# Kernel optimization log

Measured on AMD Instinct MI355X. Metric: run time of the kernel, lower is better.

Reference implementation:

```python
import jax, jax.numpy as jnp
import numpy as np

B, V, P, L, D = 8, 16, 128, 16, 128
PD = L * D  # patch_dim = patch_size * d_model = 2048


def _layernorm(x, g, b, eps=1e-5):
    mu = jnp.mean(x, axis=-1, keepdims=True)
    var = jnp.mean(jnp.square(x - mu), axis=-1, keepdims=True)
    return (x - mu) / jnp.sqrt(var + eps) * g + b


def setup_inputs() -> dict:
    key = jax.random.key(0)
    ks = jax.random.split(key, 24)
    x = jax.random.normal(ks[0], (B, V, P, L, D), jnp.float32)
    m = jax.random.randint(ks[1], (B, V, V), 0, 2) > 0
    var_mask = m & ~jnp.eye(V, dtype=bool)[None]  # keep self-attention unmasked

    def lin_w(k, fan_in, fan_out):
        return jax.random.normal(k, (fan_in, fan_out), jnp.float32) * (1.0 / np.sqrt(fan_in))

    inp = {"x": x, "var_mask": var_mask}
    # Attn_PatchLevel (attn1): query / shared kv / out projections
    inp["w_q1"] = lin_w(ks[2], PD, PD); inp["b_q1"] = jnp.zeros((PD,), jnp.float32)
    inp["w_kv1"] = lin_w(ks[3], PD, PD); inp["b_kv1"] = jnp.zeros((PD,), jnp.float32)
    inp["w_o1"] = lin_w(ks[4], PD, PD); inp["b_o1"] = jnp.zeros((PD,), jnp.float32)
    # Attn_VarLevel (attn2)
    inp["w_q2"] = lin_w(ks[5], PD, PD); inp["b_q2"] = jnp.zeros((PD,), jnp.float32)
    inp["w_kv2"] = lin_w(ks[6], PD, PD); inp["b_kv2"] = jnp.zeros((PD,), jnp.float32)
    inp["w_o2"] = lin_w(ks[7], PD, PD); inp["b_o2"] = jnp.zeros((PD,), jnp.float32)
    # LayerNorms
    inp["g1"] = jnp.ones((PD,), jnp.float32); inp["be1"] = jnp.zeros((PD,), jnp.float32)
    inp["g2"] = jnp.ones((PD,), jnp.float32); inp["be2"] = jnp.zeros((PD,), jnp.float32)
    inp["g3"] = jnp.ones((PD,), jnp.float32); inp["be3"] = jnp.zeros((PD,), jnp.float32)
    # FFN
    inp["w_l1"] = lin_w(ks[8], PD, 4 * PD); inp["b_l1"] = jnp.zeros((4 * PD,), jnp.float32)
    inp["w_l2"] = lin_w(ks[9], 4 * PD, PD); inp["b_l2"] = jnp.zeros((PD,), jnp.float32)
    return inp


def reference(x, var_mask,
              w_q1, b_q1, w_kv1, b_kv1, w_o1, b_o1,
              w_q2, b_q2, w_kv2, b_kv2, w_o2, b_o2,
              g1, be1, g2, be2, g3, be3,
              w_l1, b_l1, w_l2, b_l2):
    b, v, p, l, d = x.shape
    pd = l * d
    scale = 1.0 / np.sqrt(pd)
    x = x.reshape(b, v, p, pd)

    # ---- Attn_PatchLevel (mask=None -> no masking; keys and values share kv_projection) ----
    q = x @ w_q1 + b_q1
    kv = x @ w_kv1 + b_kv1  # keys == values in the original module
    scores = jnp.einsum('bvpd,bvsd->bvps', q, kv)  # [B,V,P,P]
    attn = jax.nn.softmax(scale * scores, axis=-1)  # dropout is identity at eval
    a1 = jnp.einsum('bvps,bvsd->bvpd', attn, kv) @ w_o1 + b_o1
    x = _layernorm(x + a1, g1, be1)

    # ---- Attn_VarLevel over variables, per patch ----
    x = x.transpose(0, 2, 1, 3)  # [B,P,V,PD]
    q = x @ w_q2 + b_q2
    kv = x @ w_kv2 + b_kv2
    scores = jnp.einsum('bpvd,bprd->bpvr', q, kv)  # [B,P,V,V]
    scores = jnp.where(var_mask[:, None, :, :], -jnp.inf, scores)
    attn = jax.nn.softmax(scale * scores, axis=-1)
    a2 = jnp.einsum('bpvr,bprd->bpvd', attn, kv) @ w_o2 + b_o2
    x = _layernorm(x + a2, g2, be2)

    # ---- FFN (torch nn.GELU default = exact erf) ----
    z = jax.nn.gelu(x @ w_l1 + b_l1, approximate=False)
    x = x + z @ w_l2 + b_l2

    x_out = _layernorm(x, g3, be3).transpose(0, 2, 1, 3)  # [B,V,P,PD]
    x_next = x_out.reshape(b, v, p // 2, 2 * l, d)
    return x_out, x_next
```

## Files before the change

kernel.cpp:

```cpp
#include <hip/hip_runtime.h>
#include <math.h>


using u16   = unsigned short;
using f32x4 = __attribute__((ext_vector_type(4))) float;
using bf16x8= __attribute__((ext_vector_type(8))) __bf16;
using u16x8 = __attribute__((ext_vector_type(8))) u16;
using u16x4 = __attribute__((ext_vector_type(4))) u16;

#define NROWS 16384
#define PD    2048
#define MEMBAR asm volatile("" ::: "memory")

__device__ __forceinline__ float bf2f(u16 u) {
    unsigned v = ((unsigned)u) << 16;
    return __builtin_bit_cast(float, v);
}
__device__ __forceinline__ u16 f2bf(float f) {
    unsigned u = __builtin_bit_cast(unsigned, f);
    u += 0x7FFFu + ((u >> 16) & 1u);
    return (u16)(u >> 16);
}
__device__ __forceinline__ void gload_lds16(const void* g, void* l) {
    __builtin_amdgcn_global_load_lds((const __attribute__((address_space(1))) void*)g,
                                     (__attribute__((address_space(3))) void*)l, 16, 0, 0);
}
__device__ __forceinline__ void block_barrier() {
    MEMBAR; __builtin_amdgcn_s_barrier(); MEMBAR;
}

template<int GELU>
__global__ __launch_bounds__(512, 2)
void gemm256(const u16* __restrict__ A, int lda,
             const u16* __restrict__ B, int ldb,
             u16* __restrict__ C1, u16* __restrict__ C2, int ncut, int ldc,
             const float* __restrict__ bias1, const float* __restrict__ bias2,
             int K, int NT, int CM, int CN)
{
    __shared__ __align__(16) char smem[131072];

    const int tid  = threadIdx.x;
    const int wv   = tid >> 6;
    const int wm   = wv >> 2;
    const int wn   = wv & 3;
    const int lane = tid & 63;
    const int fr   = lane & 15;
    const int fks16= (lane >> 4) * 16;
    const int rmask= (fr & 7) << 4;
    const int kb0  = fks16 ^ rmask;
    const int kb1  = (64 + fks16) ^ rmask;

    const int xcd = blockIdx.x & 7;
    const int ii  = blockIdx.x >> 3;
    const int RY  = NT / CN;
    const int mt  = (xcd / RY) * CM + (ii / CN);
    const int nt  = (xcd % RY) * CN + (ii % CN);
    const int m0  = mt * 256;
    const int n0  = nt * 256;

    const int rsub = tid >> 3;
    const int cswE = (((tid & 7) * 16) ^ ((rsub & 7) << 4)) >> 1;
    const int waveByte = wv * 1024;

    auto stage = [&](const u16* mat, int ld, int row0, int k0, int regionByte) {
        const u16* g0 = mat + (size_t)(row0 + rsub) * ld + k0 + cswE;
        gload_lds16(g0,                   smem + regionByte + waveByte);
        gload_lds16(g0 + (size_t)ld * 64, smem + regionByte + 8192 + waveByte);
    };

    const int aRowByte = (wm * 128 + fr) * 128;
    const int bRowByte = (wn * 64 + fr) * 128;

    const int KT = K >> 6;

    stage(A, lda, m0,       0, 0);
    stage(B, ldb, n0,       0, 32768);
    stage(A, lda, m0 + 128, 0, 16384);
    stage(B, ldb, n0 + 128, 0, 49152);
    stage(B, ldb, n0,      64, 98304);
    stage(A, lda, m0,      64, 65536);
    asm volatile("s_waitcnt vmcnt(4)" ::: "memory");
    __builtin_amdgcn_s_barrier();

    bf16x8 a[4][2], b0[2][2], b1[2][2];
    f32x4  acc[8][4] = {};

    for (int t = 0; t < KT; ++t) {
        const int Ab = (t & 1) ? 65536 : 0;
        const int Bb = Ab + 32768;
        const int Ob = Ab ^ 65536;
        const bool s1 = (t + 1 < KT), s2 = (t + 2 < KT);

        #pragma unroll
        for (int mi = 0; mi < 4; ++mi) {
            const int rb = Ab + aRowByte + mi * 2048;
            a[mi][0] = *(const bf16x8*)(smem + rb + kb0);
            a[mi][1] = *(const bf16x8*)(smem + rb + kb1);
        }
        #pragma unroll
        for (int nj = 0; nj < 2; ++nj) {
            const int rb = Bb + bRowByte + nj * 2048;
            b0[nj][0] = *(const bf16x8*)(smem + rb + kb0);
            b0[nj][1] = *(const bf16x8*)(smem + rb + kb1);
        }
        #pragma unroll
        for (int nj = 0; nj < 2; ++nj) {
            const int rb = Bb + bRowByte + 4096 + nj * 2048;
            b1[nj][0] = *(const bf16x8*)(smem + rb + kb0);
            b1[nj][1] = *(const bf16x8*)(smem + rb + kb1);
        }
        if (s1) stage(B, ldb, n0 + 128, (t + 1) << 6, Ob + 49152);
        __builtin_amdgcn_s_barrier();
        __builtin_amdgcn_s_setprio(1);
        #pragma unroll
        for (int mi = 0; mi < 4; ++mi)
            #pragma unroll
            for (int nj = 0; nj < 2; ++nj) {
                acc[mi][nj] = __builtin_amdgcn_mfma_f32_16x16x32_bf16(a[mi][0], b0[nj][0], acc[mi][nj], 0, 0, 0);
                acc[mi][nj] = __builtin_amdgcn_mfma_f32_16x16x32_bf16(a[mi][1], b0[nj][1], acc[mi][nj], 0, 0, 0);
            }
        __builtin_amdgcn_s_setprio(0);
        __builtin_amdgcn_s_barrier();

        if (s1) stage(A, lda, m0 + 128, (t + 1) << 6, Ob + 16384);
        __builtin_amdgcn_s_barrier();
        __builtin_amdgcn_s_setprio(1);
        #pragma unroll
        for (int mi = 0; mi < 4; ++mi)
            #pragma unroll
            for (int nj = 0; nj < 2; ++nj) {
                acc[mi][2 + nj] = __builtin_amdgcn_mfma_f32_16x16x32_bf16(a[mi][0], b1[nj][0], acc[mi][2 + nj], 0, 0, 0);
                acc[mi][2 + nj] = __builtin_amdgcn_mfma_f32_16x16x32_bf16(a[mi][1], b1[nj][1], acc[mi][2 + nj], 0, 0, 0);
            }
        __builtin_amdgcn_s_setprio(0);
        #pragma unroll
        for (int mi = 0; mi < 4; ++mi) {
            const int rb = Ab + aRowByte + 8192 + mi * 2048;
            a[mi][0] = *(const bf16x8*)(smem + rb + kb0);
            a[mi][1] = *(const bf16x8*)(smem + rb + kb1);
        }
        __builtin_amdgcn_s_barrier();

        if (s2) stage(B, ldb, n0, (t + 2) << 6, Bb);
        __builtin_amdgcn_s_barrier();
        __builtin_amdgcn_s_setprio(1);
        #pragma unroll
        for (int mi = 0; mi < 4; ++mi)
            #pragma unroll
            for (int nj = 0; nj < 2; ++nj) {
                acc[4 + mi][nj] = __builtin_amdgcn_mfma_f32_16x16x32_bf16(a[mi][0], b0[nj][0], acc[4 + mi][nj], 0, 0, 0);
                acc[4 + mi][nj] = __builtin_amdgcn_mfma_f32_16x16x32_bf16(a[mi][1], b0[nj][1], acc[4 + mi][nj], 0, 0, 0);
            }
        __builtin_amdgcn_s_setprio(0);
        __builtin_amdgcn_s_barrier();

        if (s2) stage(A, lda, m0, (t + 2) << 6, Ab);
        __builtin_amdgcn_s_barrier();
        __builtin_amdgcn_s_setprio(1);
        #pragma unroll
        for (int mi = 0; mi < 4; ++mi)
            #pragma unroll
            for (int nj = 0; nj < 2; ++nj) {
                acc[4 + mi][2 + nj] = __builtin_amdgcn_mfma_f32_16x16x32_bf16(a[mi][0], b1[nj][0], acc[4 + mi][2 + nj], 0, 0, 0);
                acc[4 + mi][2 + nj] = __builtin_amdgcn_mfma_f32_16x16x32_bf16(a[mi][1], b1[nj][1], acc[4 + mi][2 + nj], 0, 0, 0);
            }
        __builtin_amdgcn_s_setprio(0);
        if (s2) { asm volatile("s_waitcnt vmcnt(4)" ::: "memory"); }
        else    { asm volatile("s_waitcnt vmcnt(0)" ::: "memory"); }
        __builtin_amdgcn_s_barrier();
    }

    u16* Cout; const float* bs; int ncol;
    if (n0 < ncut) { Cout = C1; bs = bias1; ncol = n0; }
    else           { Cout = C2; bs = bias2; ncol = n0 - ncut; }

    block_barrier();
    u16* lsu = (u16*)smem;
    const int lcolB = wn * 64 + fr;
    const int lrowB = wm * 128 + (lane >> 4) * 4;
    #pragma unroll
    for (int nj = 0; nj < 4; ++nj) {
        const int lcol = lcolB + nj * 16;
        const float bb = bs[ncol + lcol];
        #pragma unroll
        for (int mi = 0; mi < 8; ++mi) {
            #pragma unroll
            for (int j = 0; j < 4; ++j) {
                float v = acc[mi][nj][j] + bb;
                if constexpr (GELU) v = 0.5f * v * (1.f + erff(v * 0.70710678118f));
                lsu[(lrowB + mi * 16 + j) * 256 + lcol] = f2bf(v);
            }
        }
    }
    block_barrier();
    const int hp = tid & 31;
    const int r0 = tid >> 5;
    #pragma unroll
    for (int ps = 0; ps < 16; ++ps) {
        const int r = ps * 16 + r0;
        u16x8 v = *(const u16x8*)&lsu[r * 256 + hp * 8];
        *(u16x8*)&Cout[(size_t)(m0 + r) * ldc + ncol + hp * 8] = v;
    }
}

template<int OUTF32, int HASBIAS>
__global__ __launch_bounds__(256, 2)
void gemm_nt(const u16* __restrict__ A, long sAg, int lda,
             const u16* __restrict__ B, long sBg, int ldb,
             void* __restrict__ Cv, long sCg, int ldc,
             const float* __restrict__ bias, int K, float scale)
{
    __shared__ __align__(16) u16 lsA[128 * 32];
    __shared__ __align__(16) u16 lsB[128 * 32];

    const int tid  = threadIdx.x;
    const int w    = tid >> 6;
    const int lane = tid & 63;
    const int m0   = blockIdx.x * 128;
    const int n0   = blockIdx.y * 128;
    A += (long)blockIdx.z * sAg;
    B += (long)blockIdx.z * sBg;

    const int wr = w >> 1, wc = w & 1;
    f32x4 acc[4][4] = {};

    const int srow = lane >> 2;
    const int skc  = (lane & 3) * 8;
    const int rA0  = 32 * w + srow;
    const int rA1  = rA0 + 16;
    const size_t aoff0 = (size_t)(m0 + rA0) * lda + skc;
    const size_t aoff1 = (size_t)(m0 + rA1) * lda + skc;
    const size_t boff0 = (size_t)(n0 + rA0) * ldb + skc;
    const size_t boff1 = (size_t)(n0 + rA1) * ldb + skc;
    u16* lA0 = lsA + 1024 * w;
    u16* lA1 = lA0 + 512;
    u16* lB0 = lsB + 1024 * w;
    u16* lB1 = lB0 + 512;

    const int fr = lane & 15;
    const int fk = (lane >> 4) * 8;

    for (int k0 = 0; k0 < K; k0 += 32) {
        gload_lds16(A + aoff0 + k0, lA0);
        gload_lds16(A + aoff1 + k0, lA1);
        gload_lds16(B + boff0 + k0, lB0);
        gload_lds16(B + boff1 + k0, lB1);
        __syncthreads();

        bf16x8 af[4], bf[4];
        #pragma unroll
        for (int m = 0; m < 4; m++)
            af[m] = *(const bf16x8*)&lsA[(wr * 64 + m * 16 + fr) * 32 + fk];
        #pragma unroll
        for (int n = 0; n < 4; n++)
            bf[n] = *(const bf16x8*)&lsB[(wc * 64 + n * 16 + fr) * 32 + fk];
        #pragma unroll
        for (int m = 0; m < 4; m++)
            #pragma unroll
            for (int n = 0; n < 4; n++)
                acc[m][n] = __builtin_amdgcn_mfma_f32_16x16x32_bf16(af[m], bf[n], acc[m][n], 0, 0, 0);
        __syncthreads();
    }

    float* Cf = (float*)Cv;
    u16*   Cb = (u16*)Cv;
    const int crow0 = m0 + wr * 64 + (lane >> 4) * 4;
    const int ccol0 = n0 + wc * 64 + fr;
    const long cbase = (long)blockIdx.z * sCg;
    #pragma unroll
    for (int n = 0; n < 4; n++) {
        const int col = ccol0 + n * 16;
        float bb = 0.f;
        if constexpr (HASBIAS) bb = bias[col];
        #pragma unroll
        for (int m = 0; m < 4; m++) {
            #pragma unroll
            for (int j = 0; j < 4; j++) {
                const int row = crow0 + m * 16 + j;
                float v = acc[m][n][j] + bb;
                const long idx = cbase + (long)row * ldc + col;
                if constexpr (OUTF32) Cf[idx] = v * scale;
                else                  Cb[idx] = f2bf(v);
            }
        }
    }
}

__global__ __launch_bounds__(256, 1)
void scores_softmax_kernel(const u16* __restrict__ Q, const u16* __restrict__ KVp,
                           u16* __restrict__ P, float scale)
{
    __shared__ __align__(16) u16 lsA[128 * 32];
    __shared__ __align__(16) u16 lsB[128 * 32];
    __shared__ float SL[128][130];

    const int g = blockIdx.x;
    const u16* A = Q   + (size_t)g * 262144;
    const u16* B = KVp + (size_t)g * 262144;

    const int tid  = threadIdx.x;
    const int w    = tid >> 6;
    const int lane = tid & 63;
    const int wr = w >> 1, wc = w & 1;
    f32x4 acc[4][4] = {};

    const int srow = lane >> 2;
    const int skc  = (lane & 3) * 8;
    const int rA0  = 32 * w + srow;
    const int rA1  = rA0 + 16;
    const size_t aoff0 = (size_t)rA0 * 2048 + skc;
    const size_t aoff1 = (size_t)rA1 * 2048 + skc;
    u16* lA0 = lsA + 1024 * w;
    u16* lA1 = lA0 + 512;
    u16* lB0 = lsB + 1024 * w;
    u16* lB1 = lB0 + 512;

    const int fr = lane & 15;
    const int fk = (lane >> 4) * 8;

    for (int k0 = 0; k0 < 2048; k0 += 32) {
        gload_lds16(A + aoff0 + k0, lA0);
        gload_lds16(A + aoff1 + k0, lA1);
        gload_lds16(B + aoff0 + k0, lB0);
        gload_lds16(B + aoff1 + k0, lB1);
        __syncthreads();
        bf16x8 af[4], bf[4];
        #pragma unroll
        for (int m = 0; m < 4; m++)
            af[m] = *(const bf16x8*)&lsA[(wr * 64 + m * 16 + fr) * 32 + fk];
        #pragma unroll
        for (int n = 0; n < 4; n++)
            bf[n] = *(const bf16x8*)&lsB[(wc * 64 + n * 16 + fr) * 32 + fk];
        #pragma unroll
        for (int m = 0; m < 4; m++)
            #pragma unroll
            for (int n = 0; n < 4; n++)
                acc[m][n] = __builtin_amdgcn_mfma_f32_16x16x32_bf16(af[m], bf[n], acc[m][n], 0, 0, 0);
        __syncthreads();
    }

    const int crow0 = wr * 64 + (lane >> 4) * 4;
    const int ccol0 = wc * 64 + fr;
    #pragma unroll
    for (int n = 0; n < 4; n++)
        #pragma unroll
        for (int m = 0; m < 4; m++)
            #pragma unroll
            for (int j = 0; j < 4; j++)
                SL[crow0 + m * 16 + j][ccol0 + n * 16] = acc[m][n][j] * scale;
    __syncthreads();

    unsigned* Pout = (unsigned*)(P + (size_t)g * 16384);
    for (int r = w * 32; r < w * 32 + 32; ++r) {
        const float v0 = SL[r][lane * 2], v1 = SL[r][lane * 2 + 1];
        float mx = fmaxf(v0, v1);
        #pragma unroll
        for (int d = 1; d < 64; d <<= 1) mx = fmaxf(mx, __shfl_xor(mx, d));
        const float e0 = __expf(v0 - mx), e1 = __expf(v1 - mx);
        float sm = e0 + e1;
        #pragma unroll
        for (int d = 1; d < 64; d <<= 1) sm += __shfl_xor(sm, d);
        const float inv = 1.f / sm;
        Pout[r * 64 + lane] = (unsigned)f2bf(e0 * inv) | ((unsigned)f2bf(e1 * inv) << 16);
    }
}

__global__ __launch_bounds__(256)
void wtrans6_kernel(const float* w0, const float* w1, const float* w2,
                    const float* w3, const float* w4, const float* w5,
                    u16* o0, u16* o1, u16* o2, u16* o3, u16* o4, u16* o5)
{
    const float* ins[6]  = {w0, w1, w2, w3, w4, w5};
    u16*         outs[6] = {o0, o1, o2, o3, o4, o5};
    const float* in  = ins[blockIdx.z];
    u16*         out = outs[blockIdx.z];

    __shared__ float tile[32][33];
    const int c0 = blockIdx.x * 32, r0 = blockIdx.y * 32;
    const int tx = threadIdx.x & 31, ty = threadIdx.x >> 5;
    #pragma unroll
    for (int i = ty; i < 32; i += 8)
        tile[i][tx] = in[(size_t)(r0 + i) * 2048 + c0 + tx];
    __syncthreads();
    #pragma unroll
    for (int i = ty; i < 32; i += 8)
        out[(size_t)(c0 + i) * 2048 + r0 + tx] = f2bf(tile[tx][i]);
}

__global__ __launch_bounds__(256)
void wtrans_kernel(const float* __restrict__ in, u16* __restrict__ out, int R, int C)
{
    __shared__ float tile[32][33];
    const int c0 = blockIdx.x * 32, r0 = blockIdx.y * 32;
    const int tx = threadIdx.x & 31, ty = threadIdx.x >> 5;
    #pragma unroll
    for (int i = ty; i < 32; i += 8)
        tile[i][tx] = in[(size_t)(r0 + i) * C + c0 + tx];
    __syncthreads();
    #pragma unroll
    for (int i = ty; i < 32; i += 8)
        out[(size_t)(c0 + i) * R + r0 + tx] = f2bf(tile[tx][i]);
}

__global__ __launch_bounds__(256)
void kvtrans_kernel(const u16* __restrict__ in, u16* __restrict__ out)
{
    __shared__ u16 tile[32][33];
    const int g = blockIdx.z;
    const int n0 = blockIdx.x * 32, m0 = blockIdx.y * 32;
    const int tx = threadIdx.x & 31, ty = threadIdx.x >> 5;
    #pragma unroll
    for (int i = ty; i < 32; i += 8)
        tile[i][tx] = in[(size_t)(g * 128 + m0 + i) * 2048 + n0 + tx];
    __syncthreads();
    #pragma unroll
    for (int i = ty; i < 32; i += 8)
        out[(size_t)g * 262144 + (size_t)(n0 + i) * 128 + m0 + tx] = tile[tx][i];
}

__global__ __launch_bounds__(256)
void cvt_f32_bf16(const float* __restrict__ in, u16* __restrict__ out)
{
    const long i = ((long)blockIdx.x * 256 + threadIdx.x) * 4;
    float4 v = *(const float4*)(in + i);
    u16x4 o;
    o[0] = f2bf(v.x); o[1] = f2bf(v.y); o[2] = f2bf(v.z); o[3] = f2bf(v.w);
    *(u16x4*)(out + i) = o;
}

template<int FINAL, int RESF32>
__global__ __launch_bounds__(256)
void ln_kernel(const void* __restrict__ residv, const u16* __restrict__ add,
               const float* __restrict__ gam, const float* __restrict__ bet,
               u16* __restrict__ xb, float* __restrict__ o1, float* __restrict__ o2)
{
    const long row = blockIdx.x;
    const int  t   = threadIdx.x;
    const long base = row * PD + t * 8;

    u16x8 av = *(const u16x8*)(add + base);
    float y[8];
    if constexpr (RESF32) {
        const float* resid = (const float*)residv;
        float4 r0 = *(const float4*)(resid + base);
        float4 r1 = *(const float4*)(resid + base + 4);
        y[0] = r0.x + bf2f(av[0]); y[1] = r0.y + bf2f(av[1]);
        y[2] = r0.z + bf2f(av[2]); y[3] = r0.w + bf2f(av[3]);
        y[4] = r1.x + bf2f(av[4]); y[5] = r1.y + bf2f(av[5]);
        y[6] = r1.z + bf2f(av[6]); y[7] = r1.w + bf2f(av[7]);
    } else {
        const u16* resid = (const u16*)residv;
        u16x8 rv = *(const u16x8*)(resid + base);
        #pragma unroll
        for (int j = 0; j < 8; j++) y[j] = bf2f(rv[j]) + bf2f(av[j]);
    }

    float s1 = 0.f, s2 = 0.f;
    #pragma unroll
    for (int j = 0; j < 8; j++) { s1 += y[j]; s2 += y[j] * y[j]; }
    #pragma unroll
    for (int d = 1; d < 64; d <<= 1) { s1 += __shfl_xor(s1, d); s2 += __shfl_xor(s2, d); }
    __shared__ float red[8];
    const int w = t >> 6;
    if ((t & 63) == 0) { red[w] = s1; red[4 + w] = s2; }
    __syncthreads();
    s1 = red[0] + red[1] + red[2] + red[3];
    s2 = red[4] + red[5] + red[6] + red[7];
    const float mean = s1 * (1.f / PD);
    const float var  = s2 * (1.f / PD) - mean * mean;
    const float rstd = rsqrtf(var + 1e-5f);

    float4 g0 = *(const float4*)(gam + t * 8);
    float4 g1 = *(const float4*)(gam + t * 8 + 4);
    float4 b0 = *(const float4*)(bet + t * 8);
    float4 b1 = *(const float4*)(bet + t * 8 + 4);
    float gv[8] = {g0.x, g0.y, g0.z, g0.w, g1.x, g1.y, g1.z, g1.w};
    float bv[8] = {b0.x, b0.y, b0.z, b0.w, b1.x, b1.y, b1.z, b1.w};

    float o[8];
    #pragma unroll
    for (int j = 0; j < 8; j++) o[j] = (y[j] - mean) * rstd * gv[j] + bv[j];

    if constexpr (FINAL) {
        float4 p0 = {o[0], o[1], o[2], o[3]}, p1 = {o[4], o[5], o[6], o[7]};
        *(float4*)(o1 + base) = p0; *(float4*)(o1 + base + 4) = p1;
        *(float4*)(o2 + base) = p0; *(float4*)(o2 + base + 4) = p1;
    } else {
        u16x8 ob;
        #pragma unroll
        for (int j = 0; j < 8; j++) ob[j] = f2bf(o[j]);
        *(u16x8*)(xb + base) = ob;
    }
}

__global__ void detect_mask_kernel(const unsigned char* __restrict__ m, int* __restrict__ flag)
{
    __shared__ int s;
    if (threadIdx.x == 0) s = 0;
    __syncthreads();
    int acc = 0;
    for (int i = threadIdx.x; i < 2048; i += 256)
        if (i & 3) acc |= m[i];
    if (acc) atomicOr(&s, 1);
    __syncthreads();
    if (threadIdx.x == 0) *flag = s;
}

__global__ __launch_bounds__(64)
void attn2_kernel(u16* __restrict__ Q, const u16* __restrict__ KV,
                  const void* __restrict__ mask, const int* __restrict__ mflag,
                  float scale)
{
    const int g = blockIdx.x;
    const int b = g >> 7, p = g & 127;
    const int lane = threadIdx.x;

    const size_t groupbase = ((size_t)(b * 16) * 128 + p) * PD;
    const size_t vstride   = (size_t)128 * PD;

    const int am   = lane & 15;
    const int koff = (lane >> 4) * 8;
    const u16* qp = Q  + groupbase + (size_t)am * vstride + koff;
    const u16* kp = KV + groupbase + (size_t)am * vstride + koff;

    f32x4 acc = {0.f, 0.f, 0.f, 0.f};
    for (int k0 = 0; k0 < PD; k0 += 32) {
        bf16x8 a  = *(const bf16x8*)(qp + k0);
        bf16x8 bb = *(const bf16x8*)(kp + k0);
        acc = __builtin_amdgcn_mfma_f32_16x16x32_bf16(a, bb, acc, 0, 0, 0);
    }

    const int vk = lane & 15;
    const int hi = lane >> 4;
    const int mf = *mflag;
    __shared__ float PL[16][16];
    float pv[4];
    #pragma unroll
    for (int j = 0; j < 4; j++) {
        const int vq = hi * 4 + j;
        float s = acc[j] * scale;
        const int midx = b * 256 + vq * 16 + vk;
        int msk;
        if (mf) msk = ((const unsigned char*)mask)[midx];
        else    msk = ((const int*)mask)[midx];
        if (msk) s = -1e30f;
        pv[j] = s;
    }
    #pragma unroll
    for (int j = 0; j < 4; j++) {
        float mx = pv[j];
        #pragma unroll
        for (int d = 1; d < 16; d <<= 1) mx = fmaxf(mx, __shfl_xor(mx, d));
        const float e = __expf(pv[j] - mx);
        float sm = e;
        #pragma unroll
        for (int d = 1; d < 16; d <<= 1) sm += __shfl_xor(sm, d);
        pv[j] = e / sm;
    }
    #pragma unroll
    for (int j = 0; j < 4; j++) PL[hi * 4 + j][vk] = pv[j];
    __syncthreads();

    const u16* kvr[16];
    #pragma unroll
    for (int v = 0; v < 16; v++) kvr[v] = KV + groupbase + (size_t)v * vstride;

    for (int vqt = 0; vqt < 16; vqt += 4) {
        float pr[4][16];
        #pragma unroll
        for (int q = 0; q < 4; q++)
            #pragma unroll
            for (int k = 0; k < 16; k++) pr[q][k] = PL[vqt + q][k];
        u16* o0 = Q + groupbase + (size_t)(vqt + 0) * vstride;
        u16* o1 = Q + groupbase + (size_t)(vqt + 1) * vstride;
        u16* o2 = Q + groupbase + (size_t)(vqt + 2) * vstride;
        u16* o3 = Q + groupbase + (size_t)(vqt + 3) * vstride;
        for (int n0 = 0; n0 < PD; n0 += 64) {
            const int n = n0 + lane;
            float a0 = 0.f, a1 = 0.f, a2 = 0.f, a3 = 0.f;
            #pragma unroll
            for (int k = 0; k < 16; k++) {
                const float kvv = bf2f(kvr[k][n]);
                a0 += pr[0][k] * kvv; a1 += pr[1][k] * kvv;
                a2 += pr[2][k] * kvv; a3 += pr[3][k] * kvv;
            }
            o0[n] = f2bf(a0); o1[n] = f2bf(a1); o2[n] = f2bf(a2); o3[n] = f2bf(a3);
        }
    }
}

extern "C" void kernel_launch(void* const* d_in, const int* in_sizes, int n_in,
                              void* d_out, int out_size, void* d_ws, size_t ws_size,
                              hipStream_t stream)
{
    const float* x0    = (const float*)d_in[0];
    const void*  vmask = d_in[1];
    const float* w_q1  = (const float*)d_in[2];  const float* b_q1  = (const float*)d_in[3];
    const float* w_kv1 = (const float*)d_in[4];  const float* b_kv1 = (const float*)d_in[5];
    const float* w_o1  = (const float*)d_in[6];  const float* b_o1  = (const float*)d_in[7];
    const float* w_q2  = (const float*)d_in[8];  const float* b_q2  = (const float*)d_in[9];
    const float* w_kv2 = (const float*)d_in[10]; const float* b_kv2 = (const float*)d_in[11];
    const float* w_o2  = (const float*)d_in[12]; const float* b_o2  = (const float*)d_in[13];
    const float* g1 = (const float*)d_in[14]; const float* be1 = (const float*)d_in[15];
    const float* g2 = (const float*)d_in[16]; const float* be2 = (const float*)d_in[17];
    const float* g3 = (const float*)d_in[18]; const float* be3 = (const float*)d_in[19];
    const float* w_l1 = (const float*)d_in[20]; const float* b_l1 = (const float*)d_in[21];
    const float* w_l2 = (const float*)d_in[22]; const float* b_l2 = (const float*)d_in[23];

    char* ws = (char*)d_ws;
    size_t off = 0;
    auto alloc = [&](size_t bytes) { size_t o = off; off += (bytes + 255) & ~(size_t)255; return o; };
    const size_t oWQ1  = alloc(8388608),  oWKV1 = alloc(8388608),  oWO1 = alloc(8388608);
    const size_t oWQ2  = alloc(8388608),  oWKV2 = alloc(8388608),  oWO2 = alloc(8388608);
    const size_t oWL1  = alloc(33554432), oWL2  = alloc(33554432);
    const size_t oXB   = alloc(67108864);
    const size_t oQ    = alloc(67108864);
    const size_t oKV   = alloc(67108864);
    const size_t oKVT  = alloc(67108864);
    const size_t oP1   = alloc(4194304);
    const size_t oFLAG = alloc(256);
    if (ws_size < off) return;

    u16* WQ1T = (u16*)(ws + oWQ1);  u16* WKV1T = (u16*)(ws + oWKV1); u16* WO1T = (u16*)(ws + oWO1);
    u16* WQ2T = (u16*)(ws + oWQ2);  u16* WKV2T = (u16*)(ws + oWKV2); u16* WO2T = (u16*)(ws + oWO2);
    u16* WL1T = (u16*)(ws + oWL1);  u16* WL2T  = (u16*)(ws + oWL2);
    u16* XB   = (u16*)(ws + oXB);   u16* Q     = (u16*)(ws + oQ);
    u16* KV   = (u16*)(ws + oKV);   u16* KVT   = (u16*)(ws + oKVT);
    u16* P1   = (u16*)(ws + oP1);   int* FLAG  = (int*)(ws + oFLAG);
    u16* H    = Q;
    u16* F    = KVT;

    const float scale = 0.02209708691f;
    float* out0 = (float*)d_out;
    float* out1 = out0 + (size_t)NROWS * PD;

    detect_mask_kernel<<<1, 256, 0, stream>>>((const unsigned char*)vmask, FLAG);

    wtrans6_kernel<<<dim3(64, 64, 6), 256, 0, stream>>>(w_q1, w_kv1, w_o1, w_q2, w_kv2, w_o2,
                                                        WQ1T, WKV1T, WO1T, WQ2T, WKV2T, WO2T);
    wtrans_kernel<<<dim3(256, 64), 256, 0, stream>>>(w_l1, WL1T, 2048, 8192);
    wtrans_kernel<<<dim3(64, 256), 256, 0, stream>>>(w_l2, WL2T, 8192, 2048);

    cvt_f32_bf16<<<32768, 256, 0, stream>>>(x0, XB);

    const int BIG = 1 << 30;

    gemm256<0><<<1024, 512, 0, stream>>>(XB, 2048, WQ1T, 2048, Q, KV, 2048, 2048,
                                         b_q1, b_kv1, 2048, 16, 32, 4);
    kvtrans_kernel<<<dim3(64, 4, 128), 256, 0, stream>>>(KV, KVT);
    scores_softmax_kernel<<<128, 256, 0, stream>>>(Q, KV, P1, scale);
    gemm_nt<0,0><<<dim3(1,16,128), 256, 0, stream>>>(P1, 16384, 128, KVT, 262144, 128, Q, 262144, 2048, nullptr, 128, 1.f);
    gemm256<0><<<512, 512, 0, stream>>>(Q, 2048, WO1T, 2048, KV, KV, BIG, 2048,
                                        b_o1, b_o1, 2048, 8, 32, 2);
    ln_kernel<0,1><<<NROWS, 256, 0, stream>>>(x0, KV, g1, be1, XB, nullptr, nullptr);

    gemm256<0><<<1024, 512, 0, stream>>>(XB, 2048, WQ2T, 2048, Q, KV, 2048, 2048,
                                         b_q2, b_kv2, 2048, 16, 32, 4);
    attn2_kernel<<<1024, 64, 0, stream>>>(Q, KV, vmask, FLAG, scale);
    gemm256<0><<<512, 512, 0, stream>>>(Q, 2048, WO2T, 2048, KV, KV, BIG, 2048,
                                        b_o2, b_o2, 2048, 8, 32, 2);
    ln_kernel<0,0><<<NROWS, 256, 0, stream>>>(XB, KV, g2, be2, XB, nullptr, nullptr);

    for (int c = 0; c < 2; c++) {
        const size_t rows = (size_t)c * 8192;
        gemm256<1><<<1024, 512, 0, stream>>>(XB + rows * 2048, 2048, WL1T, 2048,
                                             H, H, BIG, 8192, b_l1, b_l1, 2048, 32, 32, 4);
        gemm256<0><<<256, 512, 0, stream>>>(H, 8192, WL2T, 8192,
                                            F + rows * 2048, F + rows * 2048, BIG, 2048,
                                            b_l2, b_l2, 8192, 8, 32, 1);
    }
    ln_kernel<1,0><<<NROWS, 256, 0, stream>>>(XB, F, g3, be3, nullptr, out0, out1);
}
```

Baseline: 2.405 ms.

## Replace 256x256 GEMM with simpler 128x256 tile kernel at higher occupancy

```diff
diff --git a/kernel.cpp b/kernel.cpp
--- a/kernel.cpp
+++ b/kernel.cpp
@@ -10,7 +10,6 @@
 
 #define NROWS 16384
 #define PD    2048
-#define MEMBAR asm volatile("" ::: "memory")
 
 __device__ __forceinline__ float bf2f(u16 u) {
     unsigned v = ((unsigned)u) << 16;
@@ -25,19 +24,16 @@
     __builtin_amdgcn_global_load_lds((const __attribute__((address_space(1))) void*)g,
                                      (__attribute__((address_space(3))) void*)l, 16, 0, 0);
 }
-__device__ __forceinline__ void block_barrier() {
-    MEMBAR; __builtin_amdgcn_s_barrier(); MEMBAR;
-}
 
 template<int GELU>
-__global__ __launch_bounds__(512, 2)
-void gemm256(const u16* __restrict__ A, int lda,
-             const u16* __restrict__ B, int ldb,
-             u16* __restrict__ C1, u16* __restrict__ C2, int ncut, int ldc,
-             const float* __restrict__ bias1, const float* __restrict__ bias2,
-             int K, int NT, int CM, int CN)
-{
-    __shared__ __align__(16) char smem[131072];
+__global__ __launch_bounds__(512, 4)
+void gemm128n(const u16* __restrict__ A, int lda,
+              const u16* __restrict__ B, int ldb,
+              u16* __restrict__ C1, u16* __restrict__ C2, int ncut, int ldc,
+              const float* __restrict__ bias1, const float* __restrict__ bias2,
+              int K, int NT, int CM, int CN)
+{
+    __shared__ __align__(16) char smem[49152];
 
     const int tid  = threadIdx.x;
     const int wv   = tid >> 6;
@@ -45,161 +41,92 @@
     const int wn   = wv & 3;
     const int lane = tid & 63;
     const int fr   = lane & 15;
-    const int fks16= (lane >> 4) * 16;
-    const int rmask= (fr & 7) << 4;
-    const int kb0  = fks16 ^ rmask;
-    const int kb1  = (64 + fks16) ^ rmask;
+    const int kbyte= (((lane >> 4) ^ (fr & 3)) * 16);
 
     const int xcd = blockIdx.x & 7;
     const int ii  = blockIdx.x >> 3;
     const int RY  = NT / CN;
     const int mt  = (xcd / RY) * CM + (ii / CN);
     const int nt  = (xcd % RY) * CN + (ii % CN);
-    const int m0  = mt * 256;
+    const int m0  = mt * 128;
     const int n0  = nt * 256;
 
-    const int rsub = tid >> 3;
-    const int cswE = (((tid & 7) * 16) ^ ((rsub & 7) << 4)) >> 1;
-    const int waveByte = wv * 1024;
-
-    auto stage = [&](const u16* mat, int ld, int row0, int k0, int regionByte) {
-        const u16* g0 = mat + (size_t)(row0 + rsub) * ld + k0 + cswE;
-        gload_lds16(g0,                   smem + regionByte + waveByte);
-        gload_lds16(g0 + (size_t)ld * 64, smem + regionByte + 8192 + waveByte);
+    const int srow = tid >> 2;
+    const int sE   = ((tid & 3) ^ (srow & 3)) * 8;
+    const int wB   = wv * 1024;
+
+    auto stageA = [&](int k0, int destB) {
+        gload_lds16(A + (size_t)(m0 + srow) * lda + k0 + sE, smem + destB + wB);
     };
-
-    const int aRowByte = (wm * 128 + fr) * 128;
-    const int bRowByte = (wn * 64 + fr) * 128;
-
-    const int KT = K >> 6;
-
-    stage(A, lda, m0,       0, 0);
-    stage(B, ldb, n0,       0, 32768);
-    stage(A, lda, m0 + 128, 0, 16384);
-    stage(B, ldb, n0 + 128, 0, 49152);
-    stage(B, ldb, n0,      64, 98304);
-    stage(A, lda, m0,      64, 65536);
-    asm volatile("s_waitcnt vmcnt(4)" ::: "memory");
-    __builtin_amdgcn_s_barrier();
-
-    bf16x8 a[4][2], b0[2][2], b1[2][2];
-    f32x4  acc[8][4] = {};
+    auto stageB = [&](int k0, int destB) {
+        const u16* g = B + (size_t)(n0 + srow) * ldb + k0 + sE;
+        gload_lds16(g,                     smem + destB + wB);
+        gload_lds16(g + (size_t)128 * ldb, smem + destB + 8192 + wB);
+    };
+
+    const int KT = K >> 5;
+
+    stageA(0, 0);
+    stageB(0, 8192);
+
+    bf16x8 a[4], b[4];
+    f32x4  acc[4][4] = {};
 
     for (int t = 0; t < KT; ++t) {
-        const int Ab = (t & 1) ? 65536 : 0;
-        const int Bb = Ab + 32768;
-        const int Ob = Ab ^ 65536;
-        const bool s1 = (t + 1 < KT), s2 = (t + 2 < KT);
-
-        #pragma unroll
-        for (int mi = 0; mi < 4; ++mi) {
-            const int rb = Ab + aRowByte + mi * 2048;
-            a[mi][0] = *(const bf16x8*)(smem + rb + kb0);
-            a[mi][1] = *(const bf16x8*)(smem + rb + kb1);
-        }
-        #pragma unroll
-        for (int nj = 0; nj < 2; ++nj) {
-            const int rb = Bb + bRowByte + nj * 2048;
-            b0[nj][0] = *(const bf16x8*)(smem + rb + kb0);
-            b0[nj][1] = *(const bf16x8*)(smem + rb + kb1);
-        }
-        #pragma unroll
-        for (int nj = 0; nj < 2; ++nj) {
-            const int rb = Bb + bRowByte + 4096 + nj * 2048;
-            b1[nj][0] = *(const bf16x8*)(smem + rb + kb0);
-            b1[nj][1] = *(const bf16x8*)(smem + rb + kb1);
-        }
-        if (s1) stage(B, ldb, n0 + 128, (t + 1) << 6, Ob + 49152);
-        __builtin_amdgcn_s_barrier();
-        __builtin_amdgcn_s_setprio(1);
+        const int base  = (t & 1) ? 24576 : 0;
+        const int obase = base ^ 24576;
+        __syncthreads();
+        if (t + 1 < KT) { stageA((t + 1) << 5, obase); stageB((t + 1) << 5, obase + 8192); }
+
+        const int arb = base + (wm * 64 + fr) * 64 + kbyte;
         #pragma unroll
         for (int mi = 0; mi < 4; ++mi)
-            #pragma unroll
-            for (int nj = 0; nj < 2; ++nj) {
-                acc[mi][nj] = __builtin_amdgcn_mfma_f32_16x16x32_bf16(a[mi][0], b0[nj][0], acc[mi][nj], 0, 0, 0);
-                acc[mi][nj] = __builtin_amdgcn_mfma_f32_16x16x32_bf16(a[mi][1], b0[nj][1], acc[mi][nj], 0, 0, 0);
-            }
-        __builtin_amdgcn_s_setprio(0);
-        __builtin_amdgcn_s_barrier();
-
-        if (s1) stage(A, lda, m0 + 128, (t + 1) << 6, Ob + 16384);
-        __builtin_amdgcn_s_barrier();
-        __builtin_amdgcn_s_setprio(1);
+            a[mi] = *(const bf16x8*)(smem + arb + mi * 1024);
+        const int brb = base + 8192 + (wn * 64 + fr) * 64 + kbyte;
+        #pragma unroll
+        for (int nj = 0; nj < 4; ++nj)
+            b[nj] = *(const bf16x8*)(smem + brb + nj * 1024);
         #pragma unroll
         for (int mi = 0; mi < 4; ++mi)
             #pragma unroll
-            for (int nj = 0; nj < 2; ++nj) {
-                acc[mi][2 + nj] = __builtin_amdgcn_mfma_f32_16x16x32_bf16(a[mi][0], b1[nj][0], acc[mi][2 + nj], 0, 0, 0);
-                acc[mi][2 + nj] = __builtin_amdgcn_mfma_f32_16x16x32_bf16(a[mi][1], b1[nj][1], acc[mi][2 + nj], 0, 0, 0);
-            }
-        __builtin_amdgcn_s_setprio(0);
-        #pragma unroll
-        for (int mi = 0; mi < 4; ++mi) {
-            const int rb = Ab + aRowByte + 8192 + mi * 2048;
-            a[mi][0] = *(const bf16x8*)(smem + rb + kb0);
-            a[mi][1] = *(const bf16x8*)(smem + rb + kb1);
-        }
-        __builtin_amdgcn_s_barrier();
-
-        if (s2) stage(B, ldb, n0, (t + 2) << 6, Bb);
-        __builtin_amdgcn_s_barrier();
-        __builtin_amdgcn_s_setprio(1);
-        #pragma unroll
-        for (int mi = 0; mi < 4; ++mi)
-            #pragma unroll
-            for (int nj = 0; nj < 2; ++nj) {
-                acc[4 + mi][nj] = __builtin_amdgcn_mfma_f32_16x16x32_bf16(a[mi][0], b0[nj][0], acc[4 + mi][nj], 0, 0, 0);
-                acc[4 + mi][nj] = __builtin_amdgcn_mfma_f32_16x16x32_bf16(a[mi][1], b0[nj][1], acc[4 + mi][nj], 0, 0, 0);
-            }
-        __builtin_amdgcn_s_setprio(0);
-        __builtin_amdgcn_s_barrier();
-
-        if (s2) stage(A, lda, m0, (t + 2) << 6, Ab);
-        __builtin_amdgcn_s_barrier();
-        __builtin_amdgcn_s_setprio(1);
-        #pragma unroll
-        for (int mi = 0; mi < 4; ++mi)
-            #pragma unroll
-            for (int nj = 0; nj < 2; ++nj) {
-                acc[4 + mi][2 + nj] = __builtin_amdgcn_mfma_f32_16x16x32_bf16(a[mi][0], b1[nj][0], acc[4 + mi][2 + nj], 0, 0, 0);
-                acc[4 + mi][2 + nj] = __builtin_amdgcn_mfma_f32_16x16x32_bf16(a[mi][1], b1[nj][1], acc[4 + mi][2 + nj], 0, 0, 0);
-            }
-        __builtin_amdgcn_s_setprio(0);
-        if (s2) { asm volatile("s_waitcnt vmcnt(4)" ::: "memory"); }
-        else    { asm volatile("s_waitcnt vmcnt(0)" ::: "memory"); }
-        __builtin_amdgcn_s_barrier();
+            for (int nj = 0; nj < 4; ++nj)
+                acc[mi][nj] = __builtin_amdgcn_mfma_f32_16x16x32_bf16(a[mi], b[nj], acc[mi][nj], 0, 0, 0);
     }
 
     u16* Cout; const float* bs; int ncol;
     if (n0 < ncut) { Cout = C1; bs = bias1; ncol = n0; }
     else           { Cout = C2; bs = bias2; ncol = n0 - ncut; }
 
-    block_barrier();
     u16* lsu = (u16*)smem;
-    const int lcolB = wn * 64 + fr;
-    const int lrowB = wm * 128 + (lane >> 4) * 4;
-    #pragma unroll
-    for (int nj = 0; nj < 4; ++nj) {
-        const int lcol = lcolB + nj * 16;
-        const float bb = bs[ncol + lcol];
-        #pragma unroll
-        for (int mi = 0; mi < 8; ++mi) {
-            #pragma unroll
-            for (int j = 0; j < 4; ++j) {
-                float v = acc[mi][nj][j] + bb;
-                if constexpr (GELU) v = 0.5f * v * (1.f + erff(v * 0.70710678118f));
-                lsu[(lrowB + mi * 16 + j) * 256 + lcol] = f2bf(v);
+    const int lrow0 = (lane >> 4) * 4;
+    #pragma unroll
+    for (int p = 0; p < 2; ++p) {
+        __syncthreads();
+        if (wm == p) {
+            #pragma unroll
+            for (int nj = 0; nj < 4; ++nj) {
+                const int lcol = wn * 64 + nj * 16 + fr;
+                const float bb = bs[ncol + lcol];
+                #pragma unroll
+                for (int mi = 0; mi < 4; ++mi) {
+                    #pragma unroll
+                    for (int j = 0; j < 4; ++j) {
+                        float v = acc[mi][nj][j] + bb;
+                        if constexpr (GELU) v = 0.5f * v * (1.f + erff(v * 0.70710678118f));
+                        lsu[(mi * 16 + lrow0 + j) * 256 + lcol] = f2bf(v);
+                    }
+                }
             }
         }
-    }
-    block_barrier();
-    const int hp = tid & 31;
-    const int r0 = tid >> 5;
-    #pragma unroll
-    for (int ps = 0; ps < 16; ++ps) {
-        const int r = ps * 16 + r0;
-        u16x8 v = *(const u16x8*)&lsu[r * 256 + hp * 8];
-        *(u16x8*)&Cout[(size_t)(m0 + r) * ldc + ncol + hp * 8] = v;
+        __syncthreads();
+        const int hp = tid & 31;
+        const int r0 = tid >> 5;
+        #pragma unroll
+        for (int st = 0; st < 4; ++st) {
+            const int r = st * 16 + r0;
+            u16x8 v = *(const u16x8*)&lsu[r * 256 + hp * 8];
+            *(u16x8*)&Cout[(size_t)(m0 + p * 64 + r) * ldc + ncol + hp * 8] = v;
+        }
     }
 }
 
@@ -645,29 +572,29 @@
 
     const int BIG = 1 << 30;
 
-    gemm256<0><<<1024, 512, 0, stream>>>(XB, 2048, WQ1T, 2048, Q, KV, 2048, 2048,
-                                         b_q1, b_kv1, 2048, 16, 32, 4);
+    gemm128n<0><<<2048, 512, 0, stream>>>(XB, 2048, WQ1T, 2048, Q, KV, 2048, 2048,
+                                          b_q1, b_kv1, 2048, 16, 64, 4);
     kvtrans_kernel<<<dim3(64, 4, 128), 256, 0, stream>>>(KV, KVT);
     scores_softmax_kernel<<<128, 256, 0, stream>>>(Q, KV, P1, scale);
     gemm_nt<0,0><<<dim3(1,16,128), 256, 0, stream>>>(P1, 16384, 128, KVT, 262144, 128, Q, 262144, 2048, nullptr, 128, 1.f);
-    gemm256<0><<<512, 512, 0, stream>>>(Q, 2048, WO1T, 2048, KV, KV, BIG, 2048,
-                                        b_o1, b_o1, 2048, 8, 32, 2);
+    gemm128n<0><<<1024, 512, 0, stream>>>(Q, 2048, WO1T, 2048, KV, KV, BIG, 2048,
+                                          b_o1, b_o1, 2048, 8, 32, 4);
     ln_kernel<0,1><<<NROWS, 256, 0, stream>>>(x0, KV, g1, be1, XB, nullptr, nullptr);
 
-    gemm256<0><<<1024, 512, 0, stream>>>(XB, 2048, WQ2T, 2048, Q, KV, 2048, 2048,
-                                         b_q2, b_kv2, 2048, 16, 32, 4);
+    gemm128n<0><<<2048, 512, 0, stream>>>(XB, 2048, WQ2T, 2048, Q, KV, 2048, 2048,
+                                          b_q2, b_kv2, 2048, 16, 64, 4);
     attn2_kernel<<<1024, 64, 0, stream>>>(Q, KV, vmask, FLAG, scale);
-    gemm256<0><<<512, 512, 0, stream>>>(Q, 2048, WO2T, 2048, KV, KV, BIG, 2048,
-                                        b_o2, b_o2, 2048, 8, 32, 2);
+    gemm128n<0><<<1024, 512, 0, stream>>>(Q, 2048, WO2T, 2048, KV, KV, BIG, 2048,
+                                          b_o2, b_o2, 2048, 8, 32, 4);
     ln_kernel<0,0><<<NROWS, 256, 0, stream>>>(XB, KV, g2, be2, XB, nullptr, nullptr);
 
     for (int c = 0; c < 2; c++) {
         const size_t rows = (size_t)c * 8192;
-        gemm256<1><<<1024, 512, 0, stream>>>(XB + rows * 2048, 2048, WL1T, 2048,
-                                             H, H, BIG, 8192, b_l1, b_l1, 2048, 32, 32, 4);
-        gemm256<0><<<256, 512, 0, stream>>>(H, 8192, WL2T, 8192,
-                                            F + rows * 2048, F + rows * 2048, BIG, 2048,
-                                            b_l2, b_l2, 8192, 8, 32, 1);
+        gemm128n<1><<<2048, 512, 0, stream>>>(XB + rows * 2048, 2048, WL1T, 2048,
+                                              H, H, BIG, 8192, b_l1, b_l1, 2048, 32, 64, 4);
+        gemm128n<0><<<512, 512, 0, stream>>>(H, 8192, WL2T, 8192,
+                                             F + rows * 2048, F + rows * 2048, BIG, 2048,
+                                             b_l2, b_l2, 8192, 8, 16, 4);
     }
     ln_kernel<1,0><<<NROWS, 256, 0, stream>>>(XB, F, g3, be3, nullptr, out0, out1);
 }
```

Result: slower. 2.591 ms (+7.7%).

## Reschedule GEMM LDS fragment loads and vectorize var-level attention PV loop

Applied to the files above, without the earlier changes.

```diff
diff --git a/kernel.cpp b/kernel.cpp
--- a/kernel.cpp
+++ b/kernel.cpp
@@ -103,14 +103,10 @@
             b0[nj][0] = *(const bf16x8*)(smem + rb + kb0);
             b0[nj][1] = *(const bf16x8*)(smem + rb + kb1);
         }
-        #pragma unroll
-        for (int nj = 0; nj < 2; ++nj) {
-            const int rb = Bb + bRowByte + 4096 + nj * 2048;
-            b1[nj][0] = *(const bf16x8*)(smem + rb + kb0);
-            b1[nj][1] = *(const bf16x8*)(smem + rb + kb1);
-        }
         if (s1) stage(B, ldb, n0 + 128, (t + 1) << 6, Ob + 49152);
         __builtin_amdgcn_s_barrier();
+        asm volatile("s_waitcnt lgkmcnt(0)" ::: "memory");
+        __builtin_amdgcn_sched_barrier(0);
         __builtin_amdgcn_s_setprio(1);
         #pragma unroll
         for (int mi = 0; mi < 4; ++mi)
@@ -122,8 +118,16 @@
         __builtin_amdgcn_s_setprio(0);
         __builtin_amdgcn_s_barrier();
 
+        #pragma unroll
+        for (int nj = 0; nj < 2; ++nj) {
+            const int rb = Bb + bRowByte + 4096 + nj * 2048;
+            b1[nj][0] = *(const bf16x8*)(smem + rb + kb0);
+            b1[nj][1] = *(const bf16x8*)(smem + rb + kb1);
+        }
         if (s1) stage(A, lda, m0 + 128, (t + 1) << 6, Ob + 16384);
         __builtin_amdgcn_s_barrier();
+        asm volatile("s_waitcnt lgkmcnt(0)" ::: "memory");
+        __builtin_amdgcn_sched_barrier(0);
         __builtin_amdgcn_s_setprio(1);
         #pragma unroll
         for (int mi = 0; mi < 4; ++mi)
@@ -133,16 +137,18 @@
                 acc[mi][2 + nj] = __builtin_amdgcn_mfma_f32_16x16x32_bf16(a[mi][1], b1[nj][1], acc[mi][2 + nj], 0, 0, 0);
             }
         __builtin_amdgcn_s_setprio(0);
+        __builtin_amdgcn_s_barrier();
+
         #pragma unroll
         for (int mi = 0; mi < 4; ++mi) {
             const int rb = Ab + aRowByte + 8192 + mi * 2048;
             a[mi][0] = *(const bf16x8*)(smem + rb + kb0);
             a[mi][1] = *(const bf16x8*)(smem + rb + kb1);
         }
-        __builtin_amdgcn_s_barrier();
-
         if (s2) stage(B, ldb, n0, (t + 2) << 6, Bb);
         __builtin_amdgcn_s_barrier();
+        asm volatile("s_waitcnt lgkmcnt(0)" ::: "memory");
+        __builtin_amdgcn_sched_barrier(0);
         __builtin_amdgcn_s_setprio(1);
         #pragma unroll
         for (int mi = 0; mi < 4; ++mi)
@@ -561,30 +567,38 @@
     for (int j = 0; j < 4; j++) PL[hi * 4 + j][vk] = pv[j];
     __syncthreads();
 
-    const u16* kvr[16];
-    #pragma unroll
-    for (int v = 0; v < 16; v++) kvr[v] = KV + groupbase + (size_t)v * vstride;
-
-    for (int vqt = 0; vqt < 16; vqt += 4) {
-        float pr[4][16];
-        #pragma unroll
-        for (int q = 0; q < 4; q++)
-            #pragma unroll
-            for (int k = 0; k < 16; k++) pr[q][k] = PL[vqt + q][k];
-        u16* o0 = Q + groupbase + (size_t)(vqt + 0) * vstride;
-        u16* o1 = Q + groupbase + (size_t)(vqt + 1) * vstride;
-        u16* o2 = Q + groupbase + (size_t)(vqt + 2) * vstride;
-        u16* o3 = Q + groupbase + (size_t)(vqt + 3) * vstride;
-        for (int n0 = 0; n0 < PD; n0 += 64) {
-            const int n = n0 + lane;
-            float a0 = 0.f, a1 = 0.f, a2 = 0.f, a3 = 0.f;
-            #pragma unroll
-            for (int k = 0; k < 16; k++) {
-                const float kvv = bf2f(kvr[k][n]);
-                a0 += pr[0][k] * kvv; a1 += pr[1][k] * kvv;
-                a2 += pr[2][k] * kvv; a3 += pr[3][k] * kvv;
+    float pr[16][16];
+    #pragma unroll
+    for (int q = 0; q < 16; q++)
+        #pragma unroll
+        for (int k = 0; k < 16; k++) pr[q][k] = PL[q][k];
+
+    for (int pass = 0; pass < 4; ++pass) {
+        const int n = pass * 512 + lane * 8;
+        float accv[16][8];
+        #pragma unroll
+        for (int q = 0; q < 16; q++)
+            #pragma unroll
+            for (int e = 0; e < 8; e++) accv[q][e] = 0.f;
+        #pragma unroll
+        for (int k = 0; k < 16; k++) {
+            u16x8 kv8 = *(const u16x8*)(KV + groupbase + (size_t)k * vstride + n);
+            float kvf[8];
+            #pragma unroll
+            for (int e = 0; e < 8; e++) kvf[e] = bf2f(kv8[e]);
+            #pragma unroll
+            for (int q = 0; q < 16; q++) {
+                const float pq = pr[q][k];
+                #pragma unroll
+                for (int e = 0; e < 8; e++) accv[q][e] += pq * kvf[e];
             }
-            o0[n] = f2bf(a0); o1[n] = f2bf(a1); o2[n] = f2bf(a2); o3[n] = f2bf(a3);
+        }
+        #pragma unroll
+        for (int q = 0; q < 16; q++) {
+            u16x8 o;
+            #pragma unroll
+            for (int e = 0; e < 8; e++) o[e] = f2bf(accv[q][e]);
+            *(u16x8*)(Q + groupbase + (size_t)q * vstride + n) = o;
         }
     }
 }
```

Result: slower. 2.454 ms (+2.0%).
